# Kernel tuning notes

Hardware: AMD Instinct MI355X
Metric: run time of the kernel (lower is better)

The kernel has to match this reference:

```python
import jax, jax.numpy as jnp
import numpy as np

VOCAB = 32000


def setup_inputs() -> dict:
    key = jax.random.key(0)
    k1, k2, k3, k4, k5 = jax.random.split(key, 5)
    B, H, DEC_T, ATTN_LEN, D = 16, 12, 128, 512, 768
    return {
        "dec_output": jax.random.normal(k1, (B, DEC_T, D), dtype=jnp.float32),
        "final_output": jax.random.normal(k2, (B, DEC_T, VOCAB), dtype=jnp.float32),
        "attention_weights": jax.random.normal(k3, (B, H, DEC_T, ATTN_LEN), dtype=jnp.float32),
        "encoder_input": jax.random.randint(k4, (B, ATTN_LEN), 0, VOCAB, dtype=jnp.int32),
        "W_pg": jax.random.normal(k5, (D, 1), dtype=jnp.float32) / np.sqrt(D),
        "b_pg": jnp.zeros((1,), dtype=jnp.float32),
    }


def reference(dec_output, final_output, attention_weights, encoder_input, W_pg, b_pg):
    # p_gen: Dense(1) + sigmoid  -> [B, dec_t, 1]
    p_gen = jax.nn.sigmoid(dec_output @ W_pg + b_pg)

    vocab_dist = jax.nn.softmax(final_output, axis=-1)          # [B, dec_t, V]

    # mean_attention_heads=True: average over the heads axis
    attn_mean = jnp.mean(attention_weights, axis=1)              # [B, dec_t, attn_len]
    attn_dist = jax.nn.softmax(attn_mean, axis=-1)

    vocab_dists = p_gen * vocab_dist
    attn_dists = (1.0 - p_gen) * attn_dist

    dec_t = attn_dist.shape[1]

    # Per-example scatter-add of attention mass onto vocab ids.
    # For each batch b: proj[t, encoder_input[b, j]] += attn_dists[b, t, j]
    def scatter_one(ids, a):  # ids: [attn_len] int, a: [dec_t, attn_len]
        return jnp.zeros((dec_t, VOCAB), dtype=a.dtype).at[:, ids].add(a)

    attn_dists_projected = jax.vmap(scatter_one)(encoder_input, attn_dists)

    final_dists = attn_dists_projected + vocab_dists
    return jnp.log(final_dists)
```

## Files before the change

### kernel.cpp

```cpp
#include <hip/hip_runtime.h>
#include <math.h>

#define VOCAB 32000
#define NB 16
#define NH 12
#define DEC_T 128
#define ALEN 512
#define DD 768
#define NT 512
#define NW 8
#define V4 8000
#define CHUNKS 16
#define HSZ 1024
#define HMASK (HSZ - 1)
#define BMW (VOCAB / 32)
#define HEMPTY 0xFFFFFFFFu

__device__ inline float wave_sum(float v) {
#pragma unroll
  for (int o = 32; o > 0; o >>= 1) v += __shfl_down(v, o, 64);
  return v;
}
__device__ inline float wave_max(float v) {
#pragma unroll
  for (int o = 32; o > 0; o >>= 1) v = fmaxf(v, __shfl_down(v, o, 64));
  return v;
}

__global__ __launch_bounds__(NT, 4) void pg_kernel(
    const float* __restrict__ dec, const float* __restrict__ fo,
    const float* __restrict__ attnw, const int* __restrict__ ids,
    const float* __restrict__ Wpg, const float* __restrict__ bpg,
    float* __restrict__ out) {
  __shared__ unsigned s_bm[BMW];
  __shared__ unsigned s_key[HSZ];
  __shared__ float    s_val[HSZ];
  __shared__ float    s_redA[NW];
  __shared__ float    s_redB[NW];
  __shared__ float    s_redC[NW];
  __shared__ float    s_redD[NW];
  __shared__ float    s_redE[NW];

  const int bt = blockIdx.x;
  const int b = bt / DEC_T;
  const int t = bt - b * DEC_T;
  const int tid = threadIdx.x;
  const int lane = tid & 63;
  const int wid = tid >> 6;

  const float* ap = attnw + ((size_t)b * NH * DEC_T + t) * ALEN + tid;
  float hsum = 0.f;
#pragma unroll
  for (int h = 0; h < NH; ++h) hsum += ap[(size_t)h * DEC_T * ALEN];
  float pp = dec[(size_t)bt * DD + tid] * Wpg[tid];
  if (tid < DD - NT) pp += dec[(size_t)bt * DD + NT + tid] * Wpg[NT + tid];
  const unsigned myid = (unsigned)ids[b * ALEN + tid];

  const float4* row4 = (const float4*)(fo + (size_t)bt * VOCAB);
  float4 r[CHUNKS];
#pragma unroll
  for (int c = 0; c < CHUNKS; ++c) {
    int idx = c * NT + tid;
    if (idx < V4) r[c] = row4[idx];
  }

  for (int i = tid; i < BMW; i += NT) s_bm[i] = 0u;
  for (int i = tid; i < HSZ; i += NT) { s_key[i] = HEMPTY; s_val[i] = 0.f; }

  const float amean = hsum * (1.f / NH);
  float am = wave_max(amean);
  if (lane == 0) s_redA[wid] = am;
  pp = wave_sum(pp);
  if (lane == 0) s_redB[wid] = pp;
  __syncthreads();

  float amax = -INFINITY, pdot = 0.f;
#pragma unroll
  for (int i = 0; i < NW; ++i) {
    amax = fmaxf(amax, s_redA[i]);
    pdot += s_redB[i];
  }
  const float pgen = 1.f / (1.f + __expf(-(pdot + bpg[0])));
  const float ae = __expf(amean - amax);
  float as = wave_sum(ae);
  if (lane == 0) s_redC[wid] = as;

  atomicOr(&s_bm[myid >> 5], 1u << (myid & 31));
  {
    unsigned h = (myid * 2654435761u) >> 22;
    for (;;) {
      unsigned old = atomicCAS(&s_key[h], HEMPTY, myid);
      if (old == HEMPTY || old == myid) { atomicAdd(&s_val[h], ae); break; }
      h = (h + 1) & HMASK;
    }
  }

  float m = -INFINITY;
#pragma unroll
  for (int c = 0; c < CHUNKS; ++c) {
    int idx = c * NT + tid;
    if (idx < V4)
      m = fmaxf(m, fmaxf(fmaxf(r[c].x, r[c].y), fmaxf(r[c].z, r[c].w)));
  }
  m = wave_max(m);
  if (lane == 0) s_redD[wid] = m;
  __syncthreads();

  float asum = 0.f, fm = -INFINITY;
#pragma unroll
  for (int i = 0; i < NW; ++i) {
    asum += s_redC[i];
    fm = fmaxf(fm, s_redD[i]);
  }
  const float ainv = (1.f - pgen) / asum;
  float zs = 0.f;
#pragma unroll
  for (int c = 0; c < CHUNKS; ++c) {
    int idx = c * NT + tid;
    if (idx < V4)
      zs += __expf(r[c].x - fm) + __expf(r[c].y - fm) +
            __expf(r[c].z - fm) + __expf(r[c].w - fm);
  }
  zs = wave_sum(zs);
  if (lane == 0) s_redE[wid] = zs;
  __syncthreads();

  float Z = 0.f;
#pragma unroll
  for (int i = 0; i < NW; ++i) Z += s_redE[i];
  const float invZ = 1.f / Z;
  const float C = __logf(pgen) - fm - __logf(Z);

  auto hget = [&](unsigned id) -> float {
    unsigned h = (id * 2654435761u) >> 22;
    while (s_key[h] != id) h = (h + 1) & HMASK;
    return s_val[h];
  };

  float4* out4 = (float4*)(out + (size_t)bt * VOCAB);
#pragma unroll
  for (int c = 0; c < CHUNKS; ++c) {
    int idx = c * NT + tid;
    if (idx < V4) {
      const float4 x = r[c];
      float4 o;
      const unsigned nib = (s_bm[idx >> 3] >> ((idx & 7) * 4)) & 0xFu;
      if (nib == 0u) {
        o.x = x.x + C; o.y = x.y + C; o.z = x.z + C; o.w = x.w + C;
      } else {
        const unsigned v = (unsigned)idx * 4u;
        o.x = (nib & 1u) ? __logf(pgen * __expf(x.x - fm) * invZ + hget(v + 0u) * ainv) : (x.x + C);
        o.y = (nib & 2u) ? __logf(pgen * __expf(x.y - fm) * invZ + hget(v + 1u) * ainv) : (x.y + C);
        o.z = (nib & 4u) ? __logf(pgen * __expf(x.z - fm) * invZ + hget(v + 2u) * ainv) : (x.z + C);
        o.w = (nib & 8u) ? __logf(pgen * __expf(x.w - fm) * invZ + hget(v + 3u) * ainv) : (x.w + C);
      }
      out4[idx] = o;
    }
  }
}

extern "C" void kernel_launch(void* const* d_in, const int* in_sizes, int n_in,
                              void* d_out, int out_size, void* d_ws, size_t ws_size,
                              hipStream_t stream) {
  (void)in_sizes; (void)n_in; (void)out_size; (void)d_ws; (void)ws_size;
  const float* dec   = (const float*)d_in[0];
  const float* fo    = (const float*)d_in[1];
  const float* attnw = (const float*)d_in[2];
  const int*   ids   = (const int*)  d_in[3];
  const float* Wpg   = (const float*)d_in[4];
  const float* bpg   = (const float*)d_in[5];
  float* out = (float*)d_out;

  pg_kernel<<<NB * DEC_T, NT, 0, stream>>>(dec, fo, attnw, ids, Wpg, bpg, out);
}
```

Measured before the change: 513.1 us.

## Stream vocab row three times from memory instead of caching in registers

```diff
diff --git a/kernel.cpp b/kernel.cpp
--- a/kernel.cpp
+++ b/kernel.cpp
@@ -7,10 +7,9 @@
 #define DEC_T 128
 #define ALEN 512
 #define DD 768
-#define NT 512
-#define NW 8
+#define NT 256
+#define NW 4
 #define V4 8000
-#define CHUNKS 16
 #define HSZ 1024
 #define HMASK (HSZ - 1)
 #define BMW (VOCAB / 32)
@@ -38,8 +37,8 @@
   __shared__ float    s_redA[NW];
   __shared__ float    s_redB[NW];
   __shared__ float    s_redC[NW];
-  __shared__ float    s_redD[NW];
-  __shared__ float    s_redE[NW];
+  __shared__ float    s_redM[NW];
+  __shared__ float    s_redZ[NW];
 
   const int bt = blockIdx.x;
   const int b = bt / DEC_T;
@@ -48,86 +47,90 @@
   const int lane = tid & 63;
   const int wid = tid >> 6;
 
-  const float* ap = attnw + ((size_t)b * NH * DEC_T + t) * ALEN + tid;
-  float hsum = 0.f;
+  const float* ap = attnw + ((size_t)b * NH * DEC_T + t) * ALEN;
+  float h0 = 0.f, h1 = 0.f;
 #pragma unroll
-  for (int h = 0; h < NH; ++h) hsum += ap[(size_t)h * DEC_T * ALEN];
-  float pp = dec[(size_t)bt * DD + tid] * Wpg[tid];
-  if (tid < DD - NT) pp += dec[(size_t)bt * DD + NT + tid] * Wpg[NT + tid];
-  const unsigned myid = (unsigned)ids[b * ALEN + tid];
-
-  const float4* row4 = (const float4*)(fo + (size_t)bt * VOCAB);
-  float4 r[CHUNKS];
-#pragma unroll
-  for (int c = 0; c < CHUNKS; ++c) {
-    int idx = c * NT + tid;
-    if (idx < V4) r[c] = row4[idx];
+  for (int h = 0; h < NH; ++h) {
+    const float* aph = ap + (size_t)h * DEC_T * ALEN;
+    h0 += aph[tid];
+    h1 += aph[tid + NT];
   }
+  const float* dp = dec + (size_t)bt * DD;
+  float pp = dp[tid] * Wpg[tid] + dp[NT + tid] * Wpg[NT + tid] +
+             dp[2 * NT + tid] * Wpg[2 * NT + tid];
+  const unsigned id0 = (unsigned)ids[b * ALEN + tid];
+  const unsigned id1 = (unsigned)ids[b * ALEN + NT + tid];
 
   for (int i = tid; i < BMW; i += NT) s_bm[i] = 0u;
   for (int i = tid; i < HSZ; i += NT) { s_key[i] = HEMPTY; s_val[i] = 0.f; }
 
-  const float amean = hsum * (1.f / NH);
-  float am = wave_max(amean);
+  const float4* row4 = (const float4*)(fo + (size_t)bt * VOCAB);
+  float m = -INFINITY;
+  for (int i = tid; i < V4; i += NT) {
+    const float4 x = row4[i];
+    m = fmaxf(m, fmaxf(fmaxf(x.x, x.y), fmaxf(x.z, x.w)));
+  }
+  m = wave_max(m);
+  if (lane == 0) s_redM[wid] = m;
+
+  const float amean0 = h0 * (1.f / NH);
+  const float amean1 = h1 * (1.f / NH);
+  float am = wave_max(fmaxf(amean0, amean1));
   if (lane == 0) s_redA[wid] = am;
   pp = wave_sum(pp);
   if (lane == 0) s_redB[wid] = pp;
   __syncthreads();
 
-  float amax = -INFINITY, pdot = 0.f;
+  float fm = -INFINITY, amax = -INFINITY, pdot = 0.f;
 #pragma unroll
   for (int i = 0; i < NW; ++i) {
+    fm = fmaxf(fm, s_redM[i]);
     amax = fmaxf(amax, s_redA[i]);
     pdot += s_redB[i];
   }
   const float pgen = 1.f / (1.f + __expf(-(pdot + bpg[0])));
-  const float ae = __expf(amean - amax);
-  float as = wave_sum(ae);
+
+  float zs = 0.f;
+  for (int i = tid; i < V4; i += NT) {
+    const float4 x = row4[i];
+    zs += __expf(x.x - fm) + __expf(x.y - fm) +
+          __expf(x.z - fm) + __expf(x.w - fm);
+  }
+  zs = wave_sum(zs);
+  if (lane == 0) s_redZ[wid] = zs;
+
+  const float ae0 = __expf(amean0 - amax);
+  const float ae1 = __expf(amean1 - amax);
+  float as = wave_sum(ae0 + ae1);
   if (lane == 0) s_redC[wid] = as;
 
-  atomicOr(&s_bm[myid >> 5], 1u << (myid & 31));
+  atomicOr(&s_bm[id0 >> 5], 1u << (id0 & 31));
   {
-    unsigned h = (myid * 2654435761u) >> 22;
+    unsigned h = (id0 * 2654435761u) >> 22;
     for (;;) {
-      unsigned old = atomicCAS(&s_key[h], HEMPTY, myid);
-      if (old == HEMPTY || old == myid) { atomicAdd(&s_val[h], ae); break; }
+      unsigned old = atomicCAS(&s_key[h], HEMPTY, id0);
+      if (old == HEMPTY || old == id0) { atomicAdd(&s_val[h], ae0); break; }
       h = (h + 1) & HMASK;
     }
   }
-
-  float m = -INFINITY;
-#pragma unroll
-  for (int c = 0; c < CHUNKS; ++c) {
-    int idx = c * NT + tid;
-    if (idx < V4)
-      m = fmaxf(m, fmaxf(fmaxf(r[c].x, r[c].y), fmaxf(r[c].z, r[c].w)));
+  atomicOr(&s_bm[id1 >> 5], 1u << (id1 & 31));
+  {
+    unsigned h = (id1 * 2654435761u) >> 22;
+    for (;;) {
+      unsigned old = atomicCAS(&s_key[h], HEMPTY, id1);
+      if (old == HEMPTY || old == id1) { atomicAdd(&s_val[h], ae1); break; }
+      h = (h + 1) & HMASK;
+    }
   }
-  m = wave_max(m);
-  if (lane == 0) s_redD[wid] = m;
   __syncthreads();
 
-  float asum = 0.f, fm = -INFINITY;
+  float Z = 0.f, asum = 0.f;
 #pragma unroll
   for (int i = 0; i < NW; ++i) {
+    Z += s_redZ[i];
     asum += s_redC[i];
-    fm = fmaxf(fm, s_redD[i]);
   }
   const float ainv = (1.f - pgen) / asum;
-  float zs = 0.f;
-#pragma unroll
-  for (int c = 0; c < CHUNKS; ++c) {
-    int idx = c * NT + tid;
-    if (idx < V4)
-      zs += __expf(r[c].x - fm) + __expf(r[c].y - fm) +
-            __expf(r[c].z - fm) + __expf(r[c].w - fm);
-  }
-  zs = wave_sum(zs);
-  if (lane == 0) s_redE[wid] = zs;
-  __syncthreads();
-
-  float Z = 0.f;
-#pragma unroll
-  for (int i = 0; i < NW; ++i) Z += s_redE[i];
   const float invZ = 1.f / Z;
   const float C = __logf(pgen) - fm - __logf(Z);
 
@@ -138,24 +141,20 @@
   };
 
   float4* out4 = (float4*)(out + (size_t)bt * VOCAB);
-#pragma unroll
-  for (int c = 0; c < CHUNKS; ++c) {
-    int idx = c * NT + tid;
-    if (idx < V4) {
-      const float4 x = r[c];
-      float4 o;
-      const unsigned nib = (s_bm[idx >> 3] >> ((idx & 7) * 4)) & 0xFu;
-      if (nib == 0u) {
-        o.x = x.x + C; o.y = x.y + C; o.z = x.z + C; o.w = x.w + C;
-      } else {
-        const unsigned v = (unsigned)idx * 4u;
-        o.x = (nib & 1u) ? __logf(pgen * __expf(x.x - fm) * invZ + hget(v + 0u) * ainv) : (x.x + C);
-        o.y = (nib & 2u) ? __logf(pgen * __expf(x.y - fm) * invZ + hget(v + 1u) * ainv) : (x.y + C);
-        o.z = (nib & 4u) ? __logf(pgen * __expf(x.z - fm) * invZ + hget(v + 2u) * ainv) : (x.z + C);
-        o.w = (nib & 8u) ? __logf(pgen * __expf(x.w - fm) * invZ + hget(v + 3u) * ainv) : (x.w + C);
-      }
-      out4[idx] = o;
+  for (int i = tid; i < V4; i += NT) {
+    const float4 x = row4[i];
+    const unsigned nib = (s_bm[i >> 3] >> ((i & 7) * 4)) & 0xFu;
+    float4 o;
+    if (nib == 0u) {
+      o.x = x.x + C; o.y = x.y + C; o.z = x.z + C; o.w = x.w + C;
+    } else {
+      const unsigned v = (unsigned)i * 4u;
+      o.x = (nib & 1u) ? __logf(pgen * __expf(x.x - fm) * invZ + hget(v + 0u) * ainv) : (x.x + C);
+      o.y = (nib & 2u) ? __logf(pgen * __expf(x.y - fm) * invZ + hget(v + 1u) * ainv) : (x.y + C);
+      o.z = (nib & 4u) ? __logf(pgen * __expf(x.z - fm) * invZ + hget(v + 2u) * ainv) : (x.z + C);
+      o.w = (nib & 8u) ? __logf(pgen * __expf(x.w - fm) * invZ + hget(v + 3u) * ainv) : (x.w + C);
     }
+    out4[i] = o;
   }
 }
 
```

Result: slower. 556.5 us (+8.4%).
